# Kernel tuning notes

Hardware: AMD Instinct MI355X
Metric: run time of the kernel (lower is better)

Reference implementation:

```python
import jax, jax.numpy as jnp
import numpy as np
from math import factorial

AGG_NORM = 10.0

def _cg(l1, m1, l2, m2, l3, m3):
    if m3 != m1 + m2:
        return 0.0
    f = factorial
    pre = ((2*l3+1) * f(l3+l1-l2) * f(l3-l1+l2) * f(l1+l2-l3) / f(l1+l2+l3+1)) ** 0.5
    pre *= (f(l3+m3)*f(l3-m3)*f(l1-m1)*f(l1+m1)*f(l2-m2)*f(l2+m2)) ** 0.5
    s = 0.0
    for k in range(0, l1+l2-l3+1):
        d = [k, l1+l2-l3-k, l1-m1-k, l2+m2-k, l3-l2+m1+k, l3-l1-m2+k]
        if min(d) < 0:
            continue
        s += (-1.0)**k / np.prod([float(f(x)) for x in d])
    return pre * s

def _U(l):
    U = np.zeros((2*l+1, 2*l+1), dtype=complex)
    U[l, l] = 1.0
    s2 = 2 ** -0.5
    for m in range(1, l+1):
        U[l+m, l+m] = (-1)**m * s2
        U[l+m, l-m] = s2
        U[l-m, l-m] = 1j * s2
        U[l-m, l+m] = -1j * (-1)**m * s2
    return U

def _real_w3j(l1, l2, l3):
    w = np.zeros((2*l1+1, 2*l2+1, 2*l3+1))
    for m1 in range(-l1, l1+1):
        for m2 in range(-l2, l2+1):
            m3 = -(m1+m2)
            if abs(m3) <= l3:
                w[m1+l1, m2+l2, m3+l3] = (-1.0)**(l1-l2-m3) * _cg(l1, m1, l2, m2, l3, -m3) / (2*l3+1) ** 0.5
    R = np.einsum('im,jn,ko,mno->ijk', _U(l1), _U(l2), _U(l3), w.astype(complex))
    R = R.real if np.abs(R.real).max() >= np.abs(R.imag).max() else R.imag
    return jnp.asarray((R / np.linalg.norm(R)).astype(np.float32))

_TRIPLES = [(0,0,0),(0,1,1),(0,2,2),(1,0,1),(1,1,0),(1,1,2),(1,2,1),(2,0,2),(2,1,1),(2,2,0),(2,2,2),(2,2,4)]
W3J = {t: _real_w3j(*t) for t in _TRIPLES}
PATHS1 = [(0,0,0),(0,1,1),(0,2,2)]
PATHS2 = [(0,0,0),(0,1,1),(0,2,2),(1,0,1),(1,1,0),(1,1,2),(1,2,1),(2,0,2),(2,1,1),(2,2,0),(2,2,2)]
PATHS_P = [(0,0,0),(0,2,2),(2,0,2),(2,2,0),(2,2,2)]
PATHS_4 = [(0,0,0),(2,2,0),(0,2,2),(2,0,2),(2,2,2),(2,2,4)]

def _cart_basis():
    # 21-dim orthonormal basis of rank-4 tensors with ijkl=ijlk=jikl=klij symmetry
    pairs = [(0,0),(1,1),(2,2),(1,2),(0,2),(0,1)]
    mats = []
    for i, j in pairs:
        A = np.zeros((3,3)); A[i,j] = 1.0; A[j,i] = 1.0
        mats.append(A / np.linalg.norm(A))
    B = []
    for a in range(6):
        for b in range(a, 6):
            T = 0.5*(np.einsum('ij,kl->ijkl', mats[a], mats[b]) + np.einsum('ij,kl->ijkl', mats[b], mats[a]))
            B.append(T / np.linalg.norm(T))
    return jnp.asarray(np.stack(B).astype(np.float32))
B21 = _cart_basis()
_MI = np.array([0,1,2,1,0,0]); _MJ = np.array([0,1,2,2,2,1])
_MF = jnp.asarray(np.array([1,1,1,2**0.5,2**0.5,2**0.5], dtype=np.float32))

def _sh(u):
    # component-normalized real spherical harmonics, l=0..2
    x, y, z = u[:,0], u[:,1], u[:,2]
    s0 = jnp.ones_like(x)[:, None]
    s1 = 3**0.5 * u
    s2 = jnp.stack([15**0.5*x*y, 15**0.5*y*z, 5**0.5/2*(3*z*z-1), 15**0.5*x*z, 15**0.5/2*(x*x-y*y)], axis=1)
    return [s0, s1, s2]

def _gauss(x, start, end, n):
    v = jnp.linspace(start, end, n)
    step = (end - start) / (n - 1)
    return jnp.exp(-(((x[:, None] - v) / step) ** 2)) / 1.12

def _lin(x, w):
    return jnp.einsum('nck,cd->ndk', x, w)

def _interaction(xs, sh, ef, senders, receivers, n_nodes, up_w, m1, m2, lin_w, lin_b, paths, norm):
    ups = [None if x is None else _lin(x, up_w[i]) for i, x in enumerate(xs)]
    E = ef.shape[0]
    w = (jax.nn.silu(ef @ m1) @ m2).reshape(E, len(paths), -1)
    gath = {l: ups[l][senders] for l in range(len(ups)) if ups[l] is not None}
    msgs = {}
    for p, (l1, l2, l3) in enumerate(paths):
        m = jnp.einsum('eci,ej,ijk,ec->eck', gath[l1], sh[l2], W3J[(l1, l2, l3)], w[:, p, :])
        msgs[l3] = msgs[l3] + m if l3 in msgs else m
    out = []
    for l in (0, 1, 2):
        agg = jax.ops.segment_sum(msgs[l], receivers, num_segments=n_nodes) / norm
        y = _lin(agg, lin_w[l])
        if l == 0:
            y = y + lin_b[None, :, None]
        out.append(y)
    return out

def _ctp(a, b, pw):
    out = {}
    for p, (l1, l2, l3) in enumerate(PATHS_P):
        m = jnp.einsum('gci,gcj,ijk,c->gck', a[l1], b[l2], W3J[(l1, l2, l3)], pw[p])
        out[l3] = out[l3] + m if l3 in out else m
    return out

def _forward(positions, node_attrs, edge_attr, shifts, W_embed, b_embed, up1_w, mlp1_w1, mlp1_w2, lin1_w, lin1_b, up2_w, mlp2_w1, mlp2_w2, lin2_w, lin2_b, ro_lin_w, ro_gate_w, ro_gate_b, ro_lin2_w, glin_w0, glin_b0, glin_w2, prod_pw2, prod_pw3, prod_lin, fo_w, edge_index, batch, num_graphs):
    N = positions.shape[0]
    senders, receivers = edge_index[0], edge_index[1]
    x0 = (node_attrs @ W_embed + b_embed)[:, :, None]            # [N,64,1]
    vec = positions[receivers] - positions[senders] + shifts
    length = jnp.linalg.norm(vec, axis=1, keepdims=True)
    sh = _sh(vec / (length + 1e-9))
    ef = jnp.concatenate([_gauss(length[:, 0], 0.0, 0.6, 6), _gauss(edge_attr[:, 0], 0.0, 0.03, 6)], axis=1)
    xs = _interaction([x0], sh, ef, senders, receivers, N, up1_w, mlp1_w1, mlp1_w2, lin1_w, lin1_b, PATHS1, AGG_NORM)
    xs = _interaction(xs, sh, ef, senders, receivers, N, up2_w, mlp2_w1, mlp2_w2, lin2_w, lin2_b, PATHS2, AGG_NORM)
    h = [_lin(xs[l], ro_lin_w[l]) for l in range(3)]
    gates = jax.nn.silu(xs[0][:, :, 0] @ ro_gate_w + ro_gate_b)  # [N,128]
    y0 = jax.nn.silu(h[0]); y1 = h[1] * gates[:, :64, None]; y2 = h[2] * gates[:, 64:, None]
    y = [_lin(a, ro_lin2_w[i]) for i, a in enumerate((y0, y1, y2))]
    cnt = jnp.clip(jax.ops.segment_sum(jnp.ones((N,), y[0].dtype), batch, num_segments=num_graphs), 1.0)
    g = [jax.ops.segment_sum(a, batch, num_segments=num_graphs) / cnt[:, None, None] for a in y]
    r = {0: _lin(g[0], glin_w0) + glin_b0[None, :, None], 2: _lin(g[2], glin_w2)}
    t2 = _ctp(r, r, prod_pw2)
    t3 = _ctp(t2, r, prod_pw3)
    r = {l: _lin(r[l], prod_lin[0, i]) + _lin(t2[l], prod_lin[1, i]) + _lin(t3[l], prod_lin[2, i]) for i, l in enumerate((0, 2))}
    outs = {}
    for p, (l1, l2, l3) in enumerate(PATHS_4):
        wp = fo_w[p][:, :, :1] if l3 == 4 else fo_w[p]
        m = jnp.einsum('gui,gvj,ijk,uvw->gwk', r[l1], r[l2], W3J[(l1, l2, l3)], wp)
        outs[l3] = outs[l3] + m if l3 in outs else m
    G = outs[0].shape[0]
    v = jnp.concatenate([outs[0].reshape(G, 2), outs[2].reshape(G, 10), outs[4].reshape(G, 9)], axis=1)
    stiff = jnp.einsum('ga,aijkl->gijkl', v, B21)
    C = stiff[:, _MI[:, None], _MJ[:, None], _MI[None, :], _MJ[None, :]] * (_MF[:, None] * _MF[None, :])
    return C @ C  # matrix_func = 'square'

def setup_inputs():
    k = jax.random.split(jax.random.key(0), 32)
    N, E, G, C = 20000, 200000, 128, 64
    s = lambda i, shape, sc=1.0: jax.random.normal(k[i], shape, dtype=jnp.float32) * sc
    return {
        'positions': jax.random.uniform(k[0], (N, 3), dtype=jnp.float32),
        'node_attrs': jax.random.uniform(k[1], (N, 1), dtype=jnp.float32),
        'edge_attr': jax.random.uniform(k[2], (E, 1), dtype=jnp.float32) * 0.03,
        'shifts': jnp.zeros((E, 3), jnp.float32),
        'W_embed': s(5, (1, C)),
        'b_embed': jnp.zeros((C,), jnp.float32),
        'up1_w': s(6, (1, C, C), C**-0.5),
        'mlp1_w1': s(7, (12, C), 12**-0.5),
        'mlp1_w2': s(8, (C, 3 * C), C**-0.5),
        'lin1_w': s(9, (3, C, C), C**-0.5),
        'lin1_b': jnp.zeros((C,), jnp.float32),
        'up2_w': s(10, (3, C, C), C**-0.5),
        'mlp2_w1': s(11, (12, C), 12**-0.5),
        'mlp2_w2': s(12, (C, 11 * C), C**-0.5),
        'lin2_w': s(13, (3, C, C), C**-0.5),
        'lin2_b': jnp.zeros((C,), jnp.float32),
        'ro_lin_w': s(14, (3, C, C), C**-0.5),
        'ro_gate_w': s(15, (C, 2 * C), C**-0.5),
        'ro_gate_b': jnp.zeros((2 * C,), jnp.float32),
        'ro_lin2_w': s(16, (3, C, C), C**-0.5),
        'glin_w0': s(17, (C, 16), C**-0.5),
        'glin_b0': jnp.zeros((16,), jnp.float32),
        'glin_w2': s(18, (C, 16), C**-0.5),
        'prod_pw2': s(19, (5, 16), 0.5),
        'prod_pw3': s(20, (5, 16), 0.5),
        'prod_lin': s(21, (3, 2, 16, 16), 0.25),
        'fo_w': s(22, (6, 16, 16, 2), 0.25),
        'edge_index': jax.random.randint(k[3], (2, E), 0, N),
        'batch': jnp.sort(jax.random.randint(k[4], (N,), 0, G)),
        'num_graphs': G,
    }

def reference(positions, node_attrs, edge_attr, shifts, W_embed, b_embed, up1_w, mlp1_w1, mlp1_w2, lin1_w, lin1_b, up2_w, mlp2_w1, mlp2_w2, lin2_w, lin2_b, ro_lin_w, ro_gate_w, ro_gate_b, ro_lin2_w, glin_w0, glin_b0, glin_w2, prod_pw2, prod_pw3, prod_lin, fo_w, edge_index, batch, num_graphs):
    return _forward(positions, node_attrs, edge_attr, shifts, W_embed, b_embed, up1_w, mlp1_w1, mlp1_w2, lin1_w, lin1_b, up2_w, mlp2_w1, mlp2_w2, lin2_w, lin2_b, ro_lin_w, ro_gate_w, ro_gate_b, ro_lin2_w, glin_w0, glin_b0, glin_w2, prod_pw2, prod_pw3, prod_lin, fo_w, edge_index, batch, num_graphs)
```

## Files before the change

### kernel.cpp

```cpp
#include <hip/hip_runtime.h>
#include <cmath>
#include <complex>
#include <vector>
#include <cstring>

static double hfact(int n){ double r=1; for(int i=2;i<=n;i++) r*=i; return r; }

static double hcg(int l1,int m1,int l2,int m2,int l3,int m3){
  if(m3!=m1+m2) return 0.0;
  double pre = std::sqrt((2*l3+1)*hfact(l3+l1-l2)*hfact(l3-l1+l2)*hfact(l1+l2-l3)/hfact(l1+l2+l3+1));
  pre *= std::sqrt(hfact(l3+m3)*hfact(l3-m3)*hfact(l1-m1)*hfact(l1+m1)*hfact(l2-m2)*hfact(l2+m2));
  double s=0;
  for(int k=0;k<=l1+l2-l3;k++){
    int d0=k,d1=l1+l2-l3-k,d2=l1-m1-k,d3=l2+m2-k,d4=l3-l2+m1+k,d5=l3-l1-m2+k;
    if(d0<0||d1<0||d2<0||d3<0||d4<0||d5<0) continue;
    double den=hfact(d0)*hfact(d1)*hfact(d2)*hfact(d3)*hfact(d4)*hfact(d5);
    s += ((k&1)?-1.0:1.0)/den;
  }
  return pre*s;
}

static void hU(int l, std::complex<double>* U){
  int n=2*l+1;
  for(int i=0;i<n*n;i++) U[i]=std::complex<double>(0.0,0.0);
// ... 66 lines not shown

__global__ __launch_bounds__(256) void k_prep(
  const float* __restrict__ We, const float* __restrict__ be, const float* __restrict__ up1,
  const float* __restrict__ lin1, const float* __restrict__ lin1b, const float* __restrict__ up2,
  float* __restrict__ M123, float* __restrict__ Svec, float* __restrict__ Tvec, float* __restrict__ bias2)
{
  int idx=blockIdx.x*256+threadIdx.x;
  if(idx<12288){
    int l=idx>>12, c=(idx>>6)&63, d=idx&63;
    float a=0;
    for(int k=0;k<64;k++) a+=lin1[l*4096+c*64+k]*up2[l*4096+k*64+d];
    M123[idx]=0.1f*a;
  } else if(idx<12352){
    int d=idx-12288; float a=0;
    for(int c=0;c<64;c++) a+=We[c]*up1[c*64+d];
    Svec[d]=a;
  } else if(idx<12416){
    int d=idx-12352; float a=0;
    for(int c=0;c<64;c++) a+=be[c]*up1[c*64+d];
    Tvec[d]=a;
  } else if(idx<12480){
    int d=idx-12416; float a=0;
    for(int c=0;c<64;c++) a+=lin1b[c]*up2[c*64+d];
    bias2[d]=a;
  }
}

__global__ __launch_bounds__(256) void k_shuf(
  const float* __restrict__ w2a, const float* __restrict__ w2b,
  float* __restrict__ T1, float* __restrict__ T2)
{
  int idx=blockIdx.x*256+threadIdx.x;
  if(idx<16384){
    int p=idx&3, c=(idx>>2)&63, h=idx>>8;
    T1[idx]=(p<3)? w2a[h*192+p*64+c] : 0.f;
  } else if(idx<16384+49152){
    int q=idx-16384;
    int p=q%12, c=(q/12)&63, h=q/768;
    T2[q]=(p<11)? w2b[h*704+p*64+c] : 0.f;
  }
}

__global__ __launch_bounds__(256) void k_geom(
  const float* __restrict__ pos, const float* __restrict__ shifts,
  const float* __restrict__ eattr, const int* __restrict__ eidx,
  float* __restrict__ shb, float* __restrict__ efb, float* __restrict__ Tbl,
  int E, WAll W)
{
  int e=blockIdx.x*256+threadIdx.x;
  if(e>=E) return;
  int s=eidx[e], r=eidx[E+e];
  float vx=pos[r*3+0]-pos[s*3+0]+shifts[e*3+0];
  float vy=pos[r*3+1]-pos[s*3+1]+shifts[e*3+1];
  float vz=pos[r*3+2]-pos[s*3+2]+shifts[e*3+2];
  float len=sqrtf(vx*vx+vy*vy+vz*vz);
  float inv=1.f/(len+1e-9f);
  float x=vx*inv,y=vy*inv,z=vz*inv;
  const float c3=1.7320508075688772f, c15=3.872983346207417f, c5h=1.118033988749895f, c15h=1.9364916731037085f;
  float s1[3]={c3*x, c3*y, c3*z};
  float s2[5]={c15*x*y, c15*y*z, c5h*(3.f*z*z-1.f), c15*x*z, c15h*(x*x-y*y)};
  float* sp=&shb[(size_t)e*12];
  sp[0]=1.f; sp[1]=s1[0]; sp[2]=s1[1]; sp[3]=s1[2];
  sp[4]=s2[0]; sp[5]=s2[1]; sp[6]=s2[2]; sp[7]=s2[3]; sp[8]=s2[4];
  sp[9]=0.f; sp[10]=0.f; sp[11]=0.f;
  float ea=eattr[e];
  float* fp=&efb[(size_t)e*12];
  #pragma unroll
  for(int i=0;i<6;i++){ float d=(len-0.12f*(float)i)/0.12f; fp[i]=expf(-d*d)/1.12f; }
  #pragma unroll
  for(int i=0;i<6;i++){ float d=(ea-0.006f*(float)i)/0.006f; fp[6+i]=expf(-d*d)/1.12f; }
  if(Tbl){
    float* tb=&Tbl[(size_t)e*96];
    #pragma unroll
    for(int k=0;k<3;k++) tb[k]=s1[k]*W.w011[k*4];
    tb[3]=0.f;
    #pragma unroll
    for(int k=0;k<5;k++) tb[4+k]=s2[k]*W.w022[k*6];
    tb[9]=0.f; tb[10]=0.f; tb[11]=0.f;
    #pragma unroll
    for(int i=0;i<3;i++) tb[12+i]=s1[i]*W.w110[i*4];
    tb[15]=0.f;
    #pragma unroll
    for(int i=0;i<5;i++) tb[16+i]=s2[i]*W.w220[i*6];
    tb[21]=0.f; tb[22]=0.f; tb[23]=0.f;
    #pragma unroll
    for(int i=0;i<3;i++)
      #pragma unroll
      for(int k=0;k<3;k++){ float t=0;
        #pragma unroll
        for(int j=0;j<5;j++) t+=s2[j]*W.w121[(i*5+j)*3+k];
        tb[24+i*3+k]=t; }
    tb[33]=0.f; tb[34]=0.f; tb[35]=0.f;
    #pragma unroll
    for(int i=0;i<5;i++)
      #pragma unroll
      for(int k=0;k<3;k++){ float t=0;
        #pragma unroll
        for(int j=0;j<3;j++) t+=s1[j]*W.w211[(i*3+j)*3+k];
        tb[36+i*3+k]=t; }
    tb[51]=0.f;
    #pragma unroll
    for(int i=0;i<3;i++)
      #pragma unroll
      for(int k=0;k<5;k++){ float t=0;
        #pragma unroll
        for(int j=0;j<3;j++) t+=s1[j]*W.w112[(i*3+j)*5+k];
        tb[52+i*5+k]=t; }
    tb[67]=0.f;
    #pragma unroll
    for(int i=0;i<5;i++)
      #pragma unroll
      for(int k=0;k<5;k++){ float t=0;
        #pragma unroll
        for(int j=0;j<5;j++) t+=s2[j]*W.w222[(i*5+j)*5+k];
        tb[68+i*5+k]=t; }
    tb[93]=0.f; tb[94]=0.f; tb[95]=0.f;
  }
}

template<int TBL>
__global__ __launch_bounds__(256) void k_edge1(
  const float* __restrict__ na, const float* __restrict__ SV, const float* __restrict__ TV,
  const float* __restrict__ m1, const float* __restrict__ m2T,
  const float* __restrict__ sh, const float* __restrict__ Tbl, const float* __restrict__ ef,
  const int* __restrict__ eidx, float* __restrict__ agg, int E, WAll W)
{
  int tid=threadIdx.x, lane=tid&63, wid=tid>>6;
  float m1r[12];
  #pragma unroll
  for(int k=0;k<12;k++) m1r[k]=m1[k*64+lane];
  float Sv=SV[lane], Tv=TV[lane];
  int nb=(E+7)/8;
  int gw=blockIdx.x*4+wid, nw=gridDim.x*4;
  for(int b=gw;b<nb;b+=nw){
    int e0=b*8;
    float hid[8]; float3 acc[8];
    #pragma unroll
    for(int e=0;e<8;e++){
      float h=0.f;
      if(e0+e<E){
        const float4* fp=(const float4*)(ef+(size_t)(e0+e)*12);
        float4 f0=fp[0], f1=fp[1], f2=fp[2];
        h = f0.x*m1r[0]+f0.y*m1r[1]+f0.z*m1r[2]+f0.w*m1r[3]
          + f1.x*m1r[4]+f1.y*m1r[5]+f1.z*m1r[6]+f1.w*m1r[7]
          + f2.x*m1r[8]+f2.y*m1r[9]+f2.z*m1r[10]+f2.w*m1r[11];
      }
      hid[e]=silu(h);
      acc[e]=make_float3(0,0,0);
    }
    const float* Tp = m2T + (size_t)lane*4;
    #pragma unroll 4
    for(int h=0;h<64;h++){
      float4 mv=*(const float4*)(Tp + (size_t)h*256);
      #pragma unroll
      for(int e=0;e<8;e++){
        float s=bcast(hid[e],h);
        acc[e].x+=s*mv.x; acc[e].y+=s*mv.y; acc[e].z+=s*mv.z;
      }
    }
    #pragma unroll
    for(int e=0;e<8;e++){
      int ee=e0+e;
      if(ee>=E) continue;
      int snd=eidx[ee], rcv=eidx[E+ee];
      float g0 = na[snd]*Sv + Tv;
      float* dst=&agg[(size_t)rcv*576];
      atomicAdd(&dst[lane], g0*W.w000*acc[e].x);
      if constexpr(TBL){
        const float* tb=&Tbl[(size_t)ee*96];
        #pragma unroll
        for(int k=0;k<3;k++)
          atomicAdd(&dst[(1+k)*64+lane], g0*acc[e].y*tb[k]);
        #pragma unroll
        for(int k=0;k<5;k++)
          atomicAdd(&dst[(4+k)*64+lane], g0*acc[e].z*tb[4+k]);
      } else {
        const float4* shp=(const float4*)(sh+(size_t)ee*12);
        float4 h0=shp[0], h1=shp[1], h2=shp[2];
        float s1[3]={h0.y,h0.z,h0.w};
        float s2[5]={h1.x,h1.y,h1.z,h1.w,h2.x};
        #pragma unroll
        for(int k=0;k<3;k++)
          atomicAdd(&dst[(1+k)*64+lane], g0*acc[e].y*s1[k]*W.w011[k*4]);
        #pragma unroll
        for(int k=0;k<5;k++)
          atomicAdd(&dst[(4+k)*64+lane], g0*acc[e].z*s2[k]*W.w022[k*6]);
      }
    }
  }
}

template<int TBL>
__global__ __launch_bounds__(256) void k_edge2(
  const float* __restrict__ ups2, const float* __restrict__ m1, const float* __restrict__ m2T,
  const float* __restrict__ sh, const float* __restrict__ Tbl, const float* __restrict__ ef,
  const int* __restrict__ eidx, float* __restrict__ agg, int E, WAll W)
{
  int tid=threadIdx.x, lane=tid&63, wid=tid>>6;
  float m1r[12];
  #pragma unroll
  for(int k=0;k<12;k++) m1r[k]=m1[k*64+lane];
  int nb=(E+3)/4;
  int gw=blockIdx.x*4+wid, nw=gridDim.x*4;
  for(int b=gw;b<nb;b+=nw){
    int e0=b*4;
    float hid[4]; float4 accA[4], accB[4]; float3 accC[4];
    #pragma unroll
    for(int e=0;e<4;e++){
      float h=0.f;
      if(e0+e<E){
        const float4* fp=(const float4*)(ef+(size_t)(e0+e)*12);
        float4 f0=fp[0], f1=fp[1], f2=fp[2];
        h = f0.x*m1r[0]+f0.y*m1r[1]+f0.z*m1r[2]+f0.w*m1r[3]
          + f1.x*m1r[4]+f1.y*m1r[5]+f1.z*m1r[6]+f1.w*m1r[7]
          + f2.x*m1r[8]+f2.y*m1r[9]+f2.z*m1r[10]+f2.w*m1r[11];
      }
      hid[e]=silu(h);
      accA[e]=make_float4(0,0,0,0); accB[e]=make_float4(0,0,0,0);
      accC[e]=make_float3(0,0,0);
    }
    const float* Tp = m2T + (size_t)lane*12;
    #pragma unroll 4
    for(int h=0;h<64;h++){
      const float* row = Tp + (size_t)h*768;
      float4 q0=*(const float4*)(row);
      float4 q1=*(const float4*)(row+4);
      float4 q2=*(const float4*)(row+8);
      #pragma unroll
      for(int e=0;e<4;e++){
        float s=bcast(hid[e],h);
        accA[e].x+=s*q0.x; accA[e].y+=s*q0.y; accA[e].z+=s*q0.z; accA[e].w+=s*q0.w;
        accB[e].x+=s*q1.x; accB[e].y+=s*q1.y; accB[e].z+=s*q1.z; accB[e].w+=s*q1.w;
        accC[e].x+=s*q2.x; accC[e].y+=s*q2.y; accC[e].z+=s*q2.z;
      }
    }
    #pragma unroll
    for(int e=0;e<4;e++){
      int ee=e0+e;
      if(ee>=E) continue;
      int snd=eidx[ee], rcv=eidx[E+ee];
      const float* up=&ups2[(size_t)snd*576];
      float a0=accA[e].x,a1=accA[e].y,a2=accA[e].z,a3=accA[e].w;
      float a4=accB[e].x,a5=accB[e].y,a6=accB[e].z,a7=accB[e].w;
      float a8=accC[e].x,a9=accC[e].y,a10=accC[e].z;
      float g0=up[lane];
      float g1[3], g2[5];
      #pragma unroll
      for(int i=0;i<3;i++) g1[i]=up[(1+i)*64+lane];
      #pragma unroll
      for(int i=0;i<5;i++) g2[i]=up[(4+i)*64+lane];
      float* dst=&agg[(size_t)rcv*576];
      if constexpr(TBL){
        const float* tb=&Tbl[(size_t)ee*96];
        {
          float t110 = g1[0]*tb[12]+g1[1]*tb[13]+g1[2]*tb[14];
          float t220 = g2[0]*tb[16]+g2[1]*tb[17]+g2[2]*tb[18]+g2[3]*tb[19]+g2[4]*tb[20];
          atomicAdd(&dst[lane], W.w000*g0*a0 + a4*t110 + a9*t220);
        }
        #pragma unroll
        for(int k=0;k<3;k++){
          float t121 = g1[0]*tb[24+k]+g1[1]*tb[27+k]+g1[2]*tb[30+k];
          float t211 = g2[0]*tb[36+k]+g2[1]*tb[39+k]+g2[2]*tb[42+k]+g2[3]*tb[45+k]+g2[4]*tb[48+k];
          float mk = g0*a1*tb[k] + a3*g1[k]*W.w101[k*4] + a6*t121 + a8*t211;
          atomicAdd(&dst[(1+k)*64+lane], mk);
        }
        #pragma unroll
        for(int k=0;k<5;k++){
          float t112 = g1[0]*tb[52+k]+g1[1]*tb[57+k]+g1[2]*tb[62+k];
          float t222 = g2[0]*tb[68+k]+g2[1]*tb[73+k]+g2[2]*tb[78+k]+g2[3]*tb[83+k]+g2[4]*tb[88+k];
          float mk = g0*a2*tb[4+k] + a7*g2[k]*W.w202[k*6] + a5*t112 + a10*t222;
          atomicAdd(&dst[(4+k)*64+lane], mk);
        }
      } else {
        const float4* shp=(const float4*)(sh+(size_t)ee*12);
        float4 h0=shp[0], h1=shp[1], h2=shp[2];
        float s1[3]={h0.y,h0.z,h0.w};
        float s2[5]={h1.x,h1.y,h1.z,h1.w,h2.x};
        {
          float t110 = g1[0]*s1[0]*W.w110[0]+g1[1]*s1[1]*W.w110[4]+g1[2]*s1[2]*W.w110[8];
          float t220 = 0;
          #pragma unroll
          for(int i=0;i<5;i++) t220 += g2[i]*s2[i]*W.w220[i*6];
          atomicAdd(&dst[lane], W.w000*g0*a0 + a4*t110 + a9*t220);
        }
        #pragma unroll
        for(int k=0;k<3;k++){
          float mk = g0*a1*s1[k]*W.w011[k*4];
          mk += a3*g1[k]*W.w101[k*4];
          float t=0;
          #pragma unroll
          for(int i=0;i<3;i++){ float u=0;
            #pragma unroll
            for(int j=0;j<5;j++) u+=s2[j]*W.w121[(i*5+j)*3+k];
            t+=g1[i]*u; }
          mk += a6*t;
          t=0;
          #pragma unroll
          for(int i=0;i<5;i++){ float u=0;
            #pragma unroll
            for(int j=0;j<3;j++) u+=s1[j]*W.w211[(i*3+j)*3+k];
            t+=g2[i]*u; }
          mk += a8*t;
          atomicAdd(&dst[(1+k)*64+lane], mk);
        }
        #pragma unroll
        for(int k=0;k<5;k++){
          float mk = g0*a2*s2[k]*W.w022[k*6];
          float t=0;
          #pragma unroll
          for(int i=0;i<3;i++){ float u=0;
            #pragma unroll
            for(int j=0;j<3;j++) u+=s1[j]*W.w112[(i*3+j)*5+k];
            t+=g1[i]*u; }
          mk += a5*t;
          mk += a7*g2[k]*W.w202[k*6];
          t=0;
          #pragma unroll
          for(int i=0;i<5;i++){ float u=0;
            #pragma unroll
            for(int j=0;j<5;j++) u+=s2[j]*W.w222[(i*5+j)*5+k];
            t+=g2[i]*u; }
          mk += a10*t;
          atomicAdd(&dst[(4+k)*64+lane], mk);
        }
      }
    }
  }
}

template<int MODE>
__global__ __launch_bounds__(256) void k_node(
  const float* __restrict__ X, float* __restrict__ Y,
  const float* __restrict__ Ms, const float* __restrict__ bias,
  const float* __restrict__ gates, const int* __restrict__ batch,
  int N, float scale)
{
  int kk=blockIdx.y;
  int l=(kk==0)?0:(kk<4)?1:2;
  __shared__ float Mt[64][68];
  const float* M=Ms+l*4096;
  int tid=threadIdx.x;
  for(int idx=tid;idx<4096;idx+=256){ int c=idx>>6,d=idx&63; Mt[d][c]=M[idx]; }
  __syncthreads();
  int lane=tid&63, wid=tid>>6;
  int n0=(blockIdx.x*4+wid)*4;
  float xr[4];
  #pragma unroll
  for(int t=0;t<4;t++){ int n=n0+t; xr[t]=(n<N)?X[(size_t)n*576+kk*64+lane]:0.f; }
  float acc[4]={0,0,0,0};
  for(int cb=0;cb<64;cb+=4){
    float4 mv=*(const float4*)&Mt[lane][cb];
    #pragma unroll
    for(int t=0;t<4;t++){
      acc[t]+=bcast(xr[t],cb+0)*mv.x;
      acc[t]+=bcast(xr[t],cb+1)*mv.y;
      acc[t]+=bcast(xr[t],cb+2)*mv.z;
      acc[t]+=bcast(xr[t],cb+3)*mv.w;
// ... 266 lines not shown
  const float* lin2_b=(const float*)d_in[15];
  const float* ro_lin_w=(const float*)d_in[16];
  const float* ro_gate_w=(const float*)d_in[17];
  const float* ro_gate_b=(const float*)d_in[18];
  const float* ro_lin2_w=(const float*)d_in[19];
  const float* glin_w0=(const float*)d_in[20];
  const float* glin_b0=(const float*)d_in[21];
  const float* glin_w2=(const float*)d_in[22];
  const float* prod_pw2=(const float*)d_in[23];
  const float* prod_pw3=(const float*)d_in[24];
  const float* prod_lin=(const float*)d_in[25];
  const float* fo_w=(const float*)d_in[26];
  const int* edge_index=(const int*)d_in[27];
  const int* batch=(const int*)d_in[28];
  const int N=in_sizes[1];
  const int E=in_sizes[2];
  const int G=128;
  float* out=(float*)d_out;

  float* p=(float*)d_ws;
  float* shb=p;    p+=(size_t)12*E;
  float* efb=p;    p+=(size_t)12*E;
  float* bufA=p;   p+=(size_t)N*576;
  float* bufB=p;   p+=(size_t)N*576;
  float* gatesb=p; p+=(size_t)N*128;
  float* M123=p;   p+=3*4096;
  float* Svec=p;   p+=64;
  float* Tvec=p;   p+=64;
  float* bias2=p;  p+=64;
  float* m2T1=p;   p+=16384;
  float* m2T2=p;   p+=49152;
  float* gsum=p;   p+=(size_t)G*576;
  float* cntb=p;   p+=G;
  size_t baseNeed=(size_t)(p-(float*)d_ws)*sizeof(float);
  if(baseNeed>ws_size) return;
  float* Tbl=p;
  bool useTbl = (baseNeed + (size_t)96*E*sizeof(float)) <= ws_size;
  if(!useTbl) Tbl=nullptr;

  WAll wa; Wg wg;
  {
    float t000[1],t011[9],t022[25],t101[9],t110[9],t112[45],t121[45],t202[25],t211[45],t220[25],t222[125],t224[225];
    real_w3j(0,0,0,t000); real_w3j(0,1,1,t011); real_w3j(0,2,2,t022);
    real_w3j(1,0,1,t101); real_w3j(1,1,0,t110); real_w3j(1,1,2,t112); real_w3j(1,2,1,t121);
    real_w3j(2,0,2,t202); real_w3j(2,1,1,t211); real_w3j(2,2,0,t220); real_w3j(2,2,2,t222); real_w3j(2,2,4,t224);
    wa.w000=t000[0];
    std::memcpy(wa.w011,t011,sizeof t011); std::memcpy(wa.w022,t022,sizeof t022);
    std::memcpy(wa.w101,t101,sizeof t101); std::memcpy(wa.w110,t110,sizeof t110);
    std::memcpy(wa.w112,t112,sizeof t112); std::memcpy(wa.w121,t121,sizeof t121);
    std::memcpy(wa.w202,t202,sizeof t202); std::memcpy(wa.w211,t211,sizeof t211);
    std::memcpy(wa.w220,t220,sizeof t220); std::memcpy(wa.w222,t222,sizeof t222);
    wg.w000=t000[0];
    std::memcpy(wg.w022,t022,sizeof t022); std::memcpy(wg.w202,t202,sizeof t202);
    std::memcpy(wg.w220,t220,sizeof t220); std::memcpy(wg.w222,t222,sizeof t222);
    std::memcpy(wg.w224,t224,sizeof t224);
  }

  k_prep<<<49,256,0,stream>>>(W_embed,b_embed,up1_w,lin1_w,lin1_b,up2_w,M123,Svec,Tvec,bias2);
  k_shuf<<<256,256,0,stream>>>(mlp1_w2,mlp2_w2,m2T1,m2T2);
  k_geom<<<(E+255)/256,256,0,stream>>>(positions,shifts,edge_attr,edge_index,shb,efb,Tbl,E,wa);

  hipMemsetAsync(bufA,0,(size_t)N*576*sizeof(float),stream);
  const int eblocks=1280;
  if(useTbl)
    k_edge1<1><<<eblocks,256,0,stream>>>(node_attrs,Svec,Tvec,mlp1_w1,m2T1,shb,Tbl,efb,edge_index,bufA,E,wa);
  else
    k_edge1<0><<<eblocks,256,0,stream>>>(node_attrs,Svec,Tvec,mlp1_w1,m2T1,shb,Tbl,efb,edge_index,bufA,E,wa);

  dim3 ngrid((N+15)/16,9);
  k_node<0><<<ngrid,256,0,stream>>>(bufA,bufB,M123,bias2,nullptr,nullptr,N,1.0f);

  hipMemsetAsync(bufA,0,(size_t)N*576*sizeof(float),stream);
  if(useTbl)
    k_edge2<1><<<eblocks,256,0,stream>>>(bufB,mlp2_w1,m2T2,shb,Tbl,efb,edge_index,bufA,E,wa);
  else
    k_edge2<0><<<eblocks,256,0,stream>>>(bufB,mlp2_w1,m2T2,shb,Tbl,efb,edge_index,bufA,E,wa);

  k_node<1><<<ngrid,256,0,stream>>>(bufA,bufB,lin2_w,lin2_b,nullptr,nullptr,N,0.1f);
  k_gates<<<(N+15)/16,256,0,stream>>>(bufB,ro_gate_w,ro_gate_b,gatesb,N);
  k_node<2><<<ngrid,256,0,stream>>>(bufB,bufA,ro_lin_w,nullptr,gatesb,nullptr,N,1.0f);

  hipMemsetAsync(gsum,0,((size_t)G*576+G)*sizeof(float),stream);
  k_cnt<<<(N+255)/256,256,0,stream>>>(batch,cntb,N);
  k_node<3><<<ngrid,256,0,stream>>>(bufA,gsum,ro_lin2_w,nullptr,nullptr,batch,N,1.0f);

  k_graph<<<G,256,0,stream>>>(gsum,cntb,glin_w0,glin_b0,glin_w2,prod_pw2,prod_pw3,prod_lin,fo_w,out,wg);
}
```

Baseline: 1.510 ms.

## Split second edge pass across waves by tensor-product path with LDS message staging

Replaces the table-based second edge kernel with a 192-thread version. Each block takes 8 edges. The three waves each compute one quarter-slice (4 columns) of the radial MLP output and then only the tensor-product paths that use those weights. Partial messages are combined with shared-memory atomics into an LDS buffer, which is then flushed to the global aggregation with atomics. The aim is to cut per-thread register pressure and redundant MLP work, at the cost of extra block barriers, LDS atomics and a zeroing pass per batch; the non-table fallback is kept as a separate kernel.

```diff
diff --git a/kernel.cpp b/kernel.cpp
--- a/kernel.cpp
+++ b/kernel.cpp
@@ -280,10 +280,113 @@
   }
 }
 
-template<int TBL>
-__global__ __launch_bounds__(256) void k_edge2(
+__global__ __launch_bounds__(192) void k_edge2w(
   const float* __restrict__ ups2, const float* __restrict__ m1, const float* __restrict__ m2T,
-  const float* __restrict__ sh, const float* __restrict__ Tbl, const float* __restrict__ ef,
+  const float* __restrict__ Tbl, const float* __restrict__ ef,
+  const int* __restrict__ eidx, float* __restrict__ agg, int E, WAll W)
+{
+  __shared__ float m1s[768];
+  __shared__ float msg[4608];
+  int tid=threadIdx.x, lane=tid&63, wid=tid>>6;
+  for(int i=tid;i<768;i+=192) m1s[i]=m1[i];
+  __syncthreads();
+  int nb=(E+7)/8;
+  for(int b=blockIdx.x;b<nb;b+=gridDim.x){
+    int e0=b*8;
+    for(int i=tid;i<4608;i+=192) msg[i]=0.f;
+    float hid[8]; float4 acc[8];
+    #pragma unroll
+    for(int e=0;e<8;e++){
+      float h=0.f;
+      if(e0+e<E){
+        const float4* fp=(const float4*)(ef+(size_t)(e0+e)*12);
+        float4 f0=fp[0], f1=fp[1], f2=fp[2];
+        h = f0.x*m1s[0*64+lane]+f0.y*m1s[1*64+lane]+f0.z*m1s[2*64+lane]+f0.w*m1s[3*64+lane]
+          + f1.x*m1s[4*64+lane]+f1.y*m1s[5*64+lane]+f1.z*m1s[6*64+lane]+f1.w*m1s[7*64+lane]
+          + f2.x*m1s[8*64+lane]+f2.y*m1s[9*64+lane]+f2.z*m1s[10*64+lane]+f2.w*m1s[11*64+lane];
+      }
+      hid[e]=silu(h);
+      acc[e]=make_float4(0,0,0,0);
+    }
+    const float* Tp = m2T + (size_t)lane*12 + wid*4;
+    #pragma unroll 4
+    for(int h=0;h<64;h++){
+      float4 q=*(const float4*)(Tp + (size_t)h*768);
+      #pragma unroll
+      for(int e=0;e<8;e++){
+        float s=bcast(hid[e],h);
+        acc[e].x+=s*q.x; acc[e].y+=s*q.y; acc[e].z+=s*q.z; acc[e].w+=s*q.w;
+      }
+    }
+    __syncthreads();
+    #pragma unroll
+    for(int e=0;e<8;e++){
+      int ee=e0+e;
+      if(ee>=E) continue;
+      int snd=eidx[ee];
+      const float* up=&ups2[(size_t)snd*576];
+      const float* tb=&Tbl[(size_t)ee*96];
+      float* m=&msg[e*576];
+      float ax=acc[e].x, ay=acc[e].y, az=acc[e].z, aw=acc[e].w;
+      if(wid==0){
+        float g0=up[lane];
+        float g1[3];
+        #pragma unroll
+        for(int i=0;i<3;i++) g1[i]=up[(1+i)*64+lane];
+        atomicAdd(&m[lane], W.w000*g0*ax);
+        #pragma unroll
+        for(int k=0;k<3;k++)
+          atomicAdd(&m[(1+k)*64+lane], g0*ay*tb[k] + aw*g1[k]*W.w101[k*4]);
+        #pragma unroll
+        for(int k=0;k<5;k++)
+          atomicAdd(&m[(4+k)*64+lane], g0*az*tb[4+k]);
+      } else if(wid==1){
+        float g1[3], g2[5];
+        #pragma unroll
+        for(int i=0;i<3;i++) g1[i]=up[(1+i)*64+lane];
+        #pragma unroll
+        for(int i=0;i<5;i++) g2[i]=up[(4+i)*64+lane];
+        atomicAdd(&m[lane], ax*(g1[0]*tb[12]+g1[1]*tb[13]+g1[2]*tb[14]));
+        #pragma unroll
+        for(int k=0;k<3;k++)
+          atomicAdd(&m[(1+k)*64+lane], az*(g1[0]*tb[24+k]+g1[1]*tb[27+k]+g1[2]*tb[30+k]));
+        #pragma unroll
+        for(int k=0;k<5;k++)
+          atomicAdd(&m[(4+k)*64+lane],
+            ay*(g1[0]*tb[52+k]+g1[1]*tb[57+k]+g1[2]*tb[62+k]) + aw*g2[k]*W.w202[k*6]);
+      } else {
+        float g2[5];
+        #pragma unroll
+        for(int i=0;i<5;i++) g2[i]=up[(4+i)*64+lane];
+        atomicAdd(&m[lane], ay*(g2[0]*tb[16]+g2[1]*tb[17]+g2[2]*tb[18]+g2[3]*tb[19]+g2[4]*tb[20]));
+        #pragma unroll
+        for(int k=0;k<3;k++){
+          float t=g2[0]*tb[36+k]+g2[1]*tb[39+k]+g2[2]*tb[42+k]+g2[3]*tb[45+k]+g2[4]*tb[48+k];
+          atomicAdd(&m[(1+k)*64+lane], ax*t);
+        }
+        #pragma unroll
+        for(int k=0;k<5;k++){
+          float t=g2[0]*tb[68+k]+g2[1]*tb[73+k]+g2[2]*tb[78+k]+g2[3]*tb[83+k]+g2[4]*tb[88+k];
+          atomicAdd(&m[(4+k)*64+lane], az*t);
+        }
+      }
+    }
+    __syncthreads();
+    for(int i=tid;i<4608;i+=192){
+      int e=i/576, rem=i-e*576;
+      int ee=e0+e;
+      if(ee<E){
+        int rcv=eidx[E+ee];
+        atomicAdd(&agg[(size_t)rcv*576+rem], msg[i]);
+      }
+    }
+    __syncthreads();
+  }
+}
+
+__global__ __launch_bounds__(256) void k_edge2_fb(
+  const float* __restrict__ ups2, const float* __restrict__ m1, const float* __restrict__ m2T,
+  const float* __restrict__ sh, const float* __restrict__ ef,
   const int* __restrict__ eidx, float* __restrict__ agg, int E, WAll W)
 {
   int tid=threadIdx.x, lane=tid&63, wid=tid>>6;
@@ -339,80 +442,57 @@
       for(int i=0;i<3;i++) g1[i]=up[(1+i)*64+lane];
       #pragma unroll
       for(int i=0;i<5;i++) g2[i]=up[(4+i)*64+lane];
+      const float4* shp=(const float4*)(sh+(size_t)ee*12);
+      float4 h0=shp[0], h1=shp[1], h2=shp[2];
+      float s1[3]={h0.y,h0.z,h0.w};
+      float s2[5]={h1.x,h1.y,h1.z,h1.w,h2.x};
       float* dst=&agg[(size_t)rcv*576];
-      if constexpr(TBL){
-        const float* tb=&Tbl[(size_t)ee*96];
-        {
-          float t110 = g1[0]*tb[12]+g1[1]*tb[13]+g1[2]*tb[14];
-          float t220 = g2[0]*tb[16]+g2[1]*tb[17]+g2[2]*tb[18]+g2[3]*tb[19]+g2[4]*tb[20];
-          atomicAdd(&dst[lane], W.w000*g0*a0 + a4*t110 + a9*t220);
-        }
-        #pragma unroll
-        for(int k=0;k<3;k++){
-          float t121 = g1[0]*tb[24+k]+g1[1]*tb[27+k]+g1[2]*tb[30+k];
-          float t211 = g2[0]*tb[36+k]+g2[1]*tb[39+k]+g2[2]*tb[42+k]+g2[3]*tb[45+k]+g2[4]*tb[48+k];
-          float mk = g0*a1*tb[k] + a3*g1[k]*W.w101[k*4] + a6*t121 + a8*t211;
-          atomicAdd(&dst[(1+k)*64+lane], mk);
-        }
-        #pragma unroll
-        for(int k=0;k<5;k++){
-          float t112 = g1[0]*tb[52+k]+g1[1]*tb[57+k]+g1[2]*tb[62+k];
-          float t222 = g2[0]*tb[68+k]+g2[1]*tb[73+k]+g2[2]*tb[78+k]+g2[3]*tb[83+k]+g2[4]*tb[88+k];
-          float mk = g0*a2*tb[4+k] + a7*g2[k]*W.w202[k*6] + a5*t112 + a10*t222;
-          atomicAdd(&dst[(4+k)*64+lane], mk);
-        }
-      } else {
-        const float4* shp=(const float4*)(sh+(size_t)ee*12);
-        float4 h0=shp[0], h1=shp[1], h2=shp[2];
-        float s1[3]={h0.y,h0.z,h0.w};
-        float s2[5]={h1.x,h1.y,h1.z,h1.w,h2.x};
-        {
-          float t110 = g1[0]*s1[0]*W.w110[0]+g1[1]*s1[1]*W.w110[4]+g1[2]*s1[2]*W.w110[8];
-          float t220 = 0;
+      {
+        float t110 = g1[0]*s1[0]*W.w110[0]+g1[1]*s1[1]*W.w110[4]+g1[2]*s1[2]*W.w110[8];
+        float t220 = 0;
+        #pragma unroll
+        for(int i=0;i<5;i++) t220 += g2[i]*s2[i]*W.w220[i*6];
+        atomicAdd(&dst[lane], W.w000*g0*a0 + a4*t110 + a9*t220);
+      }
+      #pragma unroll
+      for(int k=0;k<3;k++){
+        float mk = g0*a1*s1[k]*W.w011[k*4];
+        mk += a3*g1[k]*W.w101[k*4];
+        float t=0;
+        #pragma unroll
+        for(int i=0;i<3;i++){ float u=0;
           #pragma unroll
-          for(int i=0;i<5;i++) t220 += g2[i]*s2[i]*W.w220[i*6];
-          atomicAdd(&dst[lane], W.w000*g0*a0 + a4*t110 + a9*t220);
-        }
-        #pragma unroll
-        for(int k=0;k<3;k++){
-          float mk = g0*a1*s1[k]*W.w011[k*4];
-          mk += a3*g1[k]*W.w101[k*4];
-          float t=0;
+          for(int j=0;j<5;j++) u+=s2[j]*W.w121[(i*5+j)*3+k];
+          t+=g1[i]*u; }
+        mk += a6*t;
+        t=0;
+        #pragma unroll
+        for(int i=0;i<5;i++){ float u=0;
           #pragma unroll
-          for(int i=0;i<3;i++){ float u=0;
-            #pragma unroll
-            for(int j=0;j<5;j++) u+=s2[j]*W.w121[(i*5+j)*3+k];
-            t+=g1[i]*u; }
-          mk += a6*t;
-          t=0;
+          for(int j=0;j<3;j++) u+=s1[j]*W.w211[(i*3+j)*3+k];
+          t+=g2[i]*u; }
+        mk += a8*t;
+        atomicAdd(&dst[(1+k)*64+lane], mk);
+      }
+      #pragma unroll
+      for(int k=0;k<5;k++){
+        float mk = g0*a2*s2[k]*W.w022[k*6];
+        float t=0;
+        #pragma unroll
+        for(int i=0;i<3;i++){ float u=0;
           #pragma unroll
-          for(int i=0;i<5;i++){ float u=0;
-            #pragma unroll
-            for(int j=0;j<3;j++) u+=s1[j]*W.w211[(i*3+j)*3+k];
-            t+=g2[i]*u; }
-          mk += a8*t;
-          atomicAdd(&dst[(1+k)*64+lane], mk);
-        }
-        #pragma unroll
-        for(int k=0;k<5;k++){
-          float mk = g0*a2*s2[k]*W.w022[k*6];
-          float t=0;
+          for(int j=0;j<3;j++) u+=s1[j]*W.w112[(i*3+j)*5+k];
+          t+=g1[i]*u; }
+        mk += a5*t;
+        mk += a7*g2[k]*W.w202[k*6];
+        t=0;
+        #pragma unroll
+        for(int i=0;i<5;i++){ float u=0;
           #pragma unroll
-          for(int i=0;i<3;i++){ float u=0;
-            #pragma unroll
-            for(int j=0;j<3;j++) u+=s1[j]*W.w112[(i*3+j)*5+k];
-            t+=g1[i]*u; }
-          mk += a5*t;
-          mk += a7*g2[k]*W.w202[k*6];
-          t=0;
-          #pragma unroll
-          for(int i=0;i<5;i++){ float u=0;
-            #pragma unroll
-            for(int j=0;j<5;j++) u+=s2[j]*W.w222[(i*5+j)*5+k];
-            t+=g2[i]*u; }
-          mk += a10*t;
-          atomicAdd(&dst[(4+k)*64+lane], mk);
-        }
+          for(int j=0;j<5;j++) u+=s2[j]*W.w222[(i*5+j)*5+k];
+          t+=g2[i]*u; }
+        mk += a10*t;
+        atomicAdd(&dst[(4+k)*64+lane], mk);
       }
     }
   }
@@ -784,10 +864,13 @@
   k_node<0><<<ngrid,256,0,stream>>>(bufA,bufB,M123,bias2,nullptr,nullptr,N,1.0f);
 
   hipMemsetAsync(bufA,0,(size_t)N*576*sizeof(float),stream);
-  if(useTbl)
-    k_edge2<1><<<eblocks,256,0,stream>>>(bufB,mlp2_w1,m2T2,shb,Tbl,efb,edge_index,bufA,E,wa);
-  else
-    k_edge2<0><<<eblocks,256,0,stream>>>(bufB,mlp2_w1,m2T2,shb,Tbl,efb,edge_index,bufA,E,wa);
+  if(useTbl){
+    int nb=(E+7)/8;
+    int g2=nb<4096?nb:4096;
+    k_edge2w<<<g2,192,0,stream>>>(bufB,mlp2_w1,m2T2,Tbl,efb,edge_index,bufA,E,wa);
+  } else {
+    k_edge2_fb<<<1280,256,0,stream>>>(bufB,mlp2_w1,m2T2,shb,efb,edge_index,bufA,E,wa);
+  }
 
   k_node<1><<<ngrid,256,0,stream>>>(bufA,bufB,lin2_w,lin2_b,nullptr,nullptr,N,0.1f);
   k_gates<<<(N+15)/16,256,0,stream>>>(bufB,ro_gate_w,ro_gate_b,gatesb,N);
```

Measured after the change: 2.894 ms. 1.92x slower.

## Sort edges by receiver via counting sort to localize scatter atomics

Applied to the files above, without the earlier changes.

Adds a histogram, single-block scan and scatter pass that reorder edges by receiver node, then writes per-edge geometry, features and tables at the sorted positions. The edge kernels read sender and receiver from the sorted arrays, so consecutive edges in a wave hit the same destination rows, which improves cache locality of the atomics. The price is several extra small kernels, including a serial single-block scan over N, plus a scattered write pattern in k_geom. Atomic ordering within a receiver is nondeterministic, so the summation order varies between runs.

```diff
diff --git a/kernel.cpp b/kernel.cpp
--- a/kernel.cpp
+++ b/kernel.cpp
@@ -131,15 +131,59 @@
   }
 }
 
+__global__ __launch_bounds__(256) void k_hist(const int* __restrict__ eidx, int* __restrict__ hist, int E){
+  int e=blockIdx.x*256+threadIdx.x;
+  if(e<E) atomicAdd(&hist[eidx[E+e]], 1);
+}
+
+__global__ __launch_bounds__(256) void k_scan(const int* __restrict__ hist, int* __restrict__ offs, int N){
+  __shared__ int tmp[256];
+  __shared__ int carry;
+  int tid=threadIdx.x;
+  if(tid==0) carry=0;
+  __syncthreads();
+  for(int base=0;base<N;base+=256){
+    int v=(base+tid<N)? hist[base+tid]:0;
+    tmp[tid]=v;
+    __syncthreads();
+    for(int off=1;off<256;off<<=1){
+      int add=(tid>=off)? tmp[tid-off]:0;
+      __syncthreads();
+      tmp[tid]+=add;
+      __syncthreads();
+    }
+    if(base+tid<N) offs[base+tid]=tmp[tid]-v+carry;
+    __syncthreads();
+    if(tid==0) carry+=tmp[255];
+    __syncthreads();
+  }
+}
+
+__global__ __launch_bounds__(256) void k_scatter(
+  const int* __restrict__ eidx, int* __restrict__ offs,
+  int* __restrict__ posOf, int* __restrict__ sndS, int* __restrict__ rcvS, int E)
+{
+  int e=blockIdx.x*256+threadIdx.x;
+  if(e<E){
+    int r=eidx[E+e];
+    int pos=atomicAdd(&offs[r],1);
+    posOf[e]=pos;
+    sndS[pos]=eidx[e];
+    rcvS[pos]=r;
+  }
+}
+
 __global__ __launch_bounds__(256) void k_geom(
   const float* __restrict__ pos, const float* __restrict__ shifts,
   const float* __restrict__ eattr, const int* __restrict__ eidx,
+  const int* __restrict__ posOf,
   float* __restrict__ shb, float* __restrict__ efb, float* __restrict__ Tbl,
   int E, WAll W)
 {
   int e=blockIdx.x*256+threadIdx.x;
   if(e>=E) return;
   int s=eidx[e], r=eidx[E+e];
+  int ps=posOf[e];
   float vx=pos[r*3+0]-pos[s*3+0]+shifts[e*3+0];
   float vy=pos[r*3+1]-pos[s*3+1]+shifts[e*3+1];
   float vz=pos[r*3+2]-pos[s*3+2]+shifts[e*3+2];
@@ -149,18 +193,18 @@
   const float c3=1.7320508075688772f, c15=3.872983346207417f, c5h=1.118033988749895f, c15h=1.9364916731037085f;
   float s1[3]={c3*x, c3*y, c3*z};
   float s2[5]={c15*x*y, c15*y*z, c5h*(3.f*z*z-1.f), c15*x*z, c15h*(x*x-y*y)};
-  float* sp=&shb[(size_t)e*12];
+  float* sp=&shb[(size_t)ps*12];
   sp[0]=1.f; sp[1]=s1[0]; sp[2]=s1[1]; sp[3]=s1[2];
   sp[4]=s2[0]; sp[5]=s2[1]; sp[6]=s2[2]; sp[7]=s2[3]; sp[8]=s2[4];
   sp[9]=0.f; sp[10]=0.f; sp[11]=0.f;
   float ea=eattr[e];
-  float* fp=&efb[(size_t)e*12];
+  float* fp=&efb[(size_t)ps*12];
   #pragma unroll
   for(int i=0;i<6;i++){ float d=(len-0.12f*(float)i)/0.12f; fp[i]=expf(-d*d)/1.12f; }
   #pragma unroll
   for(int i=0;i<6;i++){ float d=(ea-0.006f*(float)i)/0.006f; fp[6+i]=expf(-d*d)/1.12f; }
   if(Tbl){
-    float* tb=&Tbl[(size_t)e*96];
+    float* tb=&Tbl[(size_t)ps*96];
     #pragma unroll
     for(int k=0;k<3;k++) tb[k]=s1[k]*W.w011[k*4];
     tb[3]=0.f;
@@ -213,7 +257,8 @@
   const float* __restrict__ na, const float* __restrict__ SV, const float* __restrict__ TV,
   const float* __restrict__ m1, const float* __restrict__ m2T,
   const float* __restrict__ sh, const float* __restrict__ Tbl, const float* __restrict__ ef,
-  const int* __restrict__ eidx, float* __restrict__ agg, int E, WAll W)
+  const int* __restrict__ sndS, const int* __restrict__ rcvS,
+  float* __restrict__ agg, int E, WAll W)
 {
   int tid=threadIdx.x, lane=tid&63, wid=tid>>6;
   float m1r[12];
@@ -252,7 +297,7 @@
     for(int e=0;e<8;e++){
       int ee=e0+e;
       if(ee>=E) continue;
-      int snd=eidx[ee], rcv=eidx[E+ee];
+      int snd=sndS[ee], rcv=rcvS[ee];
       float g0 = na[snd]*Sv + Tv;
       float* dst=&agg[(size_t)rcv*576];
       atomicAdd(&dst[lane], g0*W.w000*acc[e].x);
@@ -284,7 +329,8 @@
 __global__ __launch_bounds__(256) void k_edge2(
   const float* __restrict__ ups2, const float* __restrict__ m1, const float* __restrict__ m2T,
   const float* __restrict__ sh, const float* __restrict__ Tbl, const float* __restrict__ ef,
-  const int* __restrict__ eidx, float* __restrict__ agg, int E, WAll W)
+  const int* __restrict__ sndS, const int* __restrict__ rcvS,
+  float* __restrict__ agg, int E, WAll W)
 {
   int tid=threadIdx.x, lane=tid&63, wid=tid>>6;
   float m1r[12];
@@ -328,7 +374,7 @@
     for(int e=0;e<4;e++){
       int ee=e0+e;
       if(ee>=E) continue;
-      int snd=eidx[ee], rcv=eidx[E+ee];
+      int snd=sndS[ee], rcv=rcvS[ee];
       const float* up=&ups2[(size_t)snd*576];
       float a0=accA[e].x,a1=accA[e].y,a2=accA[e].z,a3=accA[e].w;
       float a4=accB[e].x,a5=accB[e].y,a6=accB[e].z,a7=accB[e].w;
@@ -745,6 +791,10 @@
   float* m2T2=p;   p+=49152;
   float* gsum=p;   p+=(size_t)G*576;
   float* cntb=p;   p+=G;
+  int* offs=(int*)p;   p+=N;
+  int* posOf=(int*)p;  p+=E;
+  int* sndS=(int*)p;   p+=E;
+  int* rcvS=(int*)p;   p+=E;
   size_t baseNeed=(size_t)(p-(float*)d_ws)*sizeof(float);
   if(baseNeed>ws_size) return;
   float* Tbl=p;
@@ -771,23 +821,30 @@
 
   k_prep<<<49,256,0,stream>>>(W_embed,b_embed,up1_w,lin1_w,lin1_b,up2_w,M123,Svec,Tvec,bias2);
   k_shuf<<<256,256,0,stream>>>(mlp1_w2,mlp2_w2,m2T1,m2T2);
-  k_geom<<<(E+255)/256,256,0,stream>>>(positions,shifts,edge_attr,edge_index,shb,efb,Tbl,E,wa);
+
+  hipMemsetAsync(offs,0,(size_t)N*sizeof(int),stream);
+  k_hist<<<(E+255)/256,256,0,stream>>>(edge_index,offs,E);
+  k_scan<<<1,256,0,stream>>>(offs,posOf,N);
+  hipMemcpyAsync(offs,posOf,(size_t)N*sizeof(int),hipMemcpyDeviceToDevice,stream);
+  k_scatter<<<(E+255)/256,256,0,stream>>>(edge_index,offs,posOf,sndS,rcvS,E);
+
+  k_geom<<<(E+255)/256,256,0,stream>>>(positions,shifts,edge_attr,edge_index,posOf,shb,efb,Tbl,E,wa);
 
   hipMemsetAsync(bufA,0,(size_t)N*576*sizeof(float),stream);
   const int eblocks=1280;
   if(useTbl)
-    k_edge1<1><<<eblocks,256,0,stream>>>(node_attrs,Svec,Tvec,mlp1_w1,m2T1,shb,Tbl,efb,edge_index,bufA,E,wa);
+    k_edge1<1><<<eblocks,256,0,stream>>>(node_attrs,Svec,Tvec,mlp1_w1,m2T1,shb,Tbl,efb,sndS,rcvS,bufA,E,wa);
   else
-    k_edge1<0><<<eblocks,256,0,stream>>>(node_attrs,Svec,Tvec,mlp1_w1,m2T1,shb,Tbl,efb,edge_index,bufA,E,wa);
+    k_edge1<0><<<eblocks,256,0,stream>>>(node_attrs,Svec,Tvec,mlp1_w1,m2T1,shb,Tbl,efb,sndS,rcvS,bufA,E,wa);
 
   dim3 ngrid((N+15)/16,9);
   k_node<0><<<ngrid,256,0,stream>>>(bufA,bufB,M123,bias2,nullptr,nullptr,N,1.0f);
 
   hipMemsetAsync(bufA,0,(size_t)N*576*sizeof(float),stream);
   if(useTbl)
-    k_edge2<1><<<eblocks,256,0,stream>>>(bufB,mlp2_w1,m2T2,shb,Tbl,efb,edge_index,bufA,E,wa);
+    k_edge2<1><<<eblocks,256,0,stream>>>(bufB,mlp2_w1,m2T2,shb,Tbl,efb,sndS,rcvS,bufA,E,wa);
   else
-    k_edge2<0><<<eblocks,256,0,stream>>>(bufB,mlp2_w1,m2T2,shb,Tbl,efb,edge_index,bufA,E,wa);
+    k_edge2<0><<<eblocks,256,0,stream>>>(bufB,mlp2_w1,m2T2,shb,Tbl,efb,sndS,rcvS,bufA,E,wa);
 
   k_node<1><<<ngrid,256,0,stream>>>(bufA,bufB,lin2_w,lin2_b,nullptr,nullptr,N,0.1f);
   k_gates<<<(N+15)/16,256,0,stream>>>(bufB,ro_gate_w,ro_gate_b,gatesb,N);
```

Result: slower. 1.626 ms (+7.7%).

## Stage edge-MLP second-layer weights through shared memory in chunks per block

Applied to the files above, without the earlier changes.

The weight-transpose layout is changed from channel-interleaved to path-major rows, so each lane reads contiguous per-path rows. In both edge kernels, the second MLP weight matrix is now copied into LDS eight hidden units at a time and shared by all four waves of the block, which now process consecutive edge groups. The first-layer weights also move from registers to LDS. This cuts redundant global and L2 weight traffic, but adds two block barriers per chunk and makes the waves of a block run in lockstep.

```diff
diff --git a/kernel.cpp b/kernel.cpp
--- a/kernel.cpp
+++ b/kernel.cpp
@@ -122,11 +122,11 @@
 {
   int idx=blockIdx.x*256+threadIdx.x;
   if(idx<16384){
-    int p=idx&3, c=(idx>>2)&63, h=idx>>8;
+    int h=idx>>8, rem=idx&255, p=rem>>6, c=rem&63;
     T1[idx]=(p<3)? w2a[h*192+p*64+c] : 0.f;
   } else if(idx<16384+49152){
     int q=idx-16384;
-    int p=q%12, c=(q/12)&63, h=q/768;
+    int h=q/768, rem=q%768, p=rem/64, c=rem&63;
     T2[q]=(p<11)? w2b[h*704+p*64+c] : 0.f;
   }
 }
@@ -215,37 +215,46 @@
   const float* __restrict__ sh, const float* __restrict__ Tbl, const float* __restrict__ ef,
   const int* __restrict__ eidx, float* __restrict__ agg, int E, WAll W)
 {
+  __shared__ __align__(16) float wl[8*256];
+  __shared__ float m1s[768];
   int tid=threadIdx.x, lane=tid&63, wid=tid>>6;
-  float m1r[12];
-  #pragma unroll
-  for(int k=0;k<12;k++) m1r[k]=m1[k*64+lane];
+  for(int i=tid;i<768;i+=256) m1s[i]=m1[i];
   float Sv=SV[lane], Tv=TV[lane];
-  int nb=(E+7)/8;
-  int gw=blockIdx.x*4+wid, nw=gridDim.x*4;
-  for(int b=gw;b<nb;b+=nw){
-    int e0=b*8;
-    float hid[8]; float3 acc[8];
+  __syncthreads();
+  int nb=(E+31)/32;
+  for(int b=blockIdx.x;b<nb;b+=gridDim.x){
+    int e0=b*32+wid*8;
+    float hid[8]; float acc[8][3];
     #pragma unroll
     for(int e=0;e<8;e++){
       float h=0.f;
       if(e0+e<E){
         const float4* fp=(const float4*)(ef+(size_t)(e0+e)*12);
         float4 f0=fp[0], f1=fp[1], f2=fp[2];
-        h = f0.x*m1r[0]+f0.y*m1r[1]+f0.z*m1r[2]+f0.w*m1r[3]
-          + f1.x*m1r[4]+f1.y*m1r[5]+f1.z*m1r[6]+f1.w*m1r[7]
-          + f2.x*m1r[8]+f2.y*m1r[9]+f2.z*m1r[10]+f2.w*m1r[11];
+        h = f0.x*m1s[0*64+lane]+f0.y*m1s[1*64+lane]+f0.z*m1s[2*64+lane]+f0.w*m1s[3*64+lane]
+          + f1.x*m1s[4*64+lane]+f1.y*m1s[5*64+lane]+f1.z*m1s[6*64+lane]+f1.w*m1s[7*64+lane]
+          + f2.x*m1s[8*64+lane]+f2.y*m1s[9*64+lane]+f2.z*m1s[10*64+lane]+f2.w*m1s[11*64+lane];
       }
       hid[e]=silu(h);
-      acc[e]=make_float3(0,0,0);
-    }
-    const float* Tp = m2T + (size_t)lane*4;
-    #pragma unroll 4
-    for(int h=0;h<64;h++){
-      float4 mv=*(const float4*)(Tp + (size_t)h*256);
-      #pragma unroll
-      for(int e=0;e<8;e++){
-        float s=bcast(hid[e],h);
-        acc[e].x+=s*mv.x; acc[e].y+=s*mv.y; acc[e].z+=s*mv.z;
+      acc[e][0]=0; acc[e][1]=0; acc[e][2]=0;
+    }
+    for(int ch=0;ch<8;ch++){
+      __syncthreads();
+      const float4* src=(const float4*)(m2T+(size_t)ch*2048);
+      float4* dst4=(float4*)wl;
+      dst4[tid]=src[tid];
+      dst4[tid+256]=src[tid+256];
+      __syncthreads();
+      #pragma unroll
+      for(int h8=0;h8<8;h8++){
+        int h=ch*8+h8;
+        const float* wr=&wl[h8*256];
+        float w0=wr[lane], w1=wr[64+lane], w2=wr[128+lane];
+        #pragma unroll
+        for(int e=0;e<8;e++){
+          float s=bcast(hid[e],h);
+          acc[e][0]+=s*w0; acc[e][1]+=s*w1; acc[e][2]+=s*w2;
+        }
       }
     }
     #pragma unroll
@@ -255,15 +264,15 @@
       int snd=eidx[ee], rcv=eidx[E+ee];
       float g0 = na[snd]*Sv + Tv;
       float* dst=&agg[(size_t)rcv*576];
-      atomicAdd(&dst[lane], g0*W.w000*acc[e].x);
+      atomicAdd(&dst[lane], g0*W.w000*acc[e][0]);
       if constexpr(TBL){
         const float* tb=&Tbl[(size_t)ee*96];
         #pragma unroll
         for(int k=0;k<3;k++)
-          atomicAdd(&dst[(1+k)*64+lane], g0*acc[e].y*tb[k]);
+          atomicAdd(&dst[(1+k)*64+lane], g0*acc[e][1]*tb[k]);
         #pragma unroll
         for(int k=0;k<5;k++)
-          atomicAdd(&dst[(4+k)*64+lane], g0*acc[e].z*tb[4+k]);
+          atomicAdd(&dst[(4+k)*64+lane], g0*acc[e][2]*tb[4+k]);
       } else {
         const float4* shp=(const float4*)(sh+(size_t)ee*12);
         float4 h0=shp[0], h1=shp[1], h2=shp[2];
@@ -271,10 +280,10 @@
         float s2[5]={h1.x,h1.y,h1.z,h1.w,h2.x};
         #pragma unroll
         for(int k=0;k<3;k++)
-          atomicAdd(&dst[(1+k)*64+lane], g0*acc[e].y*s1[k]*W.w011[k*4]);
+          atomicAdd(&dst[(1+k)*64+lane], g0*acc[e][1]*s1[k]*W.w011[k*4]);
         #pragma unroll
         for(int k=0;k<5;k++)
-          atomicAdd(&dst[(4+k)*64+lane], g0*acc[e].z*s2[k]*W.w022[k*6]);
+          atomicAdd(&dst[(4+k)*64+lane], g0*acc[e][2]*s2[k]*W.w022[k*6]);
       }
     }
   }
@@ -286,42 +295,46 @@
   const float* __restrict__ sh, const float* __restrict__ Tbl, const float* __restrict__ ef,
   const int* __restrict__ eidx, float* __restrict__ agg, int E, WAll W)
 {
+  __shared__ __align__(16) float wl[8*768];
+  __shared__ float m1s[768];
   int tid=threadIdx.x, lane=tid&63, wid=tid>>6;
-  float m1r[12];
-  #pragma unroll
-  for(int k=0;k<12;k++) m1r[k]=m1[k*64+lane];
-  int nb=(E+3)/4;
-  int gw=blockIdx.x*4+wid, nw=gridDim.x*4;
-  for(int b=gw;b<nb;b+=nw){
-    int e0=b*4;
-    float hid[4]; float4 accA[4], accB[4]; float3 accC[4];
+  for(int i=tid;i<768;i+=256) m1s[i]=m1[i];
+  __syncthreads();
+  int nb=(E+15)/16;
+  for(int b=blockIdx.x;b<nb;b+=gridDim.x){
+    int e0=b*16+wid*4;
+    float hid[4]; float acc[4][11];
     #pragma unroll
     for(int e=0;e<4;e++){
       float h=0.f;
       if(e0+e<E){
         const float4* fp=(const float4*)(ef+(size_t)(e0+e)*12);
         float4 f0=fp[0], f1=fp[1], f2=fp[2];
-        h = f0.x*m1r[0]+f0.y*m1r[1]+f0.z*m1r[2]+f0.w*m1r[3]
-          + f1.x*m1r[4]+f1.y*m1r[5]+f1.z*m1r[6]+f1.w*m1r[7]
-          + f2.x*m1r[8]+f2.y*m1r[9]+f2.z*m1r[10]+f2.w*m1r[11];
+        h = f0.x*m1s[0*64+lane]+f0.y*m1s[1*64+lane]+f0.z*m1s[2*64+lane]+f0.w*m1s[3*64+lane]
+          + f1.x*m1s[4*64+lane]+f1.y*m1s[5*64+lane]+f1.z*m1s[6*64+lane]+f1.w*m1s[7*64+lane]
+          + f2.x*m1s[8*64+lane]+f2.y*m1s[9*64+lane]+f2.z*m1s[10*64+lane]+f2.w*m1s[11*64+lane];
       }
       hid[e]=silu(h);
-      accA[e]=make_float4(0,0,0,0); accB[e]=make_float4(0,0,0,0);
-      accC[e]=make_float3(0,0,0);
-    }
-    const float* Tp = m2T + (size_t)lane*12;
-    #pragma unroll 4
-    for(int h=0;h<64;h++){
-      const float* row = Tp + (size_t)h*768;
-      float4 q0=*(const float4*)(row);
-      float4 q1=*(const float4*)(row+4);
-      float4 q2=*(const float4*)(row+8);
-      #pragma unroll
-      for(int e=0;e<4;e++){
-        float s=bcast(hid[e],h);
-        accA[e].x+=s*q0.x; accA[e].y+=s*q0.y; accA[e].z+=s*q0.z; accA[e].w+=s*q0.w;
-        accB[e].x+=s*q1.x; accB[e].y+=s*q1.y; accB[e].z+=s*q1.z; accB[e].w+=s*q1.w;
-        accC[e].x+=s*q2.x; accC[e].y+=s*q2.y; accC[e].z+=s*q2.z;
+      #pragma unroll
+      for(int p=0;p<11;p++) acc[e][p]=0.f;
+    }
+    for(int ch=0;ch<8;ch++){
+      __syncthreads();
+      const float4* src=(const float4*)(m2T+(size_t)ch*6144);
+      float4* dst4=(float4*)wl;
+      #pragma unroll
+      for(int i=0;i<6;i++) dst4[tid+i*256]=src[tid+i*256];
+      __syncthreads();
+      #pragma unroll
+      for(int h8=0;h8<8;h8++){
+        int h=ch*8+h8;
+        const float* wr=&wl[h8*768];
+        float s0=bcast(hid[0],h), s1b=bcast(hid[1],h), s2b=bcast(hid[2],h), s3b=bcast(hid[3],h);
+        #pragma unroll
+        for(int p=0;p<11;p++){
+          float w=wr[p*64+lane];
+          acc[0][p]+=s0*w; acc[1][p]+=s1b*w; acc[2][p]+=s2b*w; acc[3][p]+=s3b*w;
+        }
       }
     }
     #pragma unroll
@@ -330,9 +343,9 @@
       if(ee>=E) continue;
       int snd=eidx[ee], rcv=eidx[E+ee];
       const float* up=&ups2[(size_t)snd*576];
-      float a0=accA[e].x,a1=accA[e].y,a2=accA[e].z,a3=accA[e].w;
-      float a4=accB[e].x,a5=accB[e].y,a6=accB[e].z,a7=accB[e].w;
-      float a8=accC[e].x,a9=accC[e].y,a10=accC[e].z;
+      float a0=acc[e][0],a1=acc[e][1],a2=acc[e][2],a3=acc[e][3];
+      float a4=acc[e][4],a5=acc[e][5],a6=acc[e][6],a7=acc[e][7];
+      float a8=acc[e][8],a9=acc[e][9],a10=acc[e][10];
       float g0=up[lane];
       float g1[3], g2[5];
       #pragma unroll
```

Measured after the change: 1.457 ms. 3.5% less time.
